# Performance work log

Hardware: AMD Instinct MI355X
Metric: run time of the kernel (lower is better)

Reference implementation:

```python
import jax, jax.numpy as jnp
import numpy as np

BATCH, NODES, ENC, DEC = 8192, 1_000_000, 128, 128


def setup_inputs() -> dict:
    key = jax.random.key(0)
    k1, k2, k3, k4 = jax.random.split(key, 4)
    query = jax.random.normal(k1, (BATCH, DEC), dtype=jnp.float32)
    values = jax.random.normal(k2, (NODES, ENC), dtype=jnp.float32)
    index = jax.random.randint(k3, (NODES,), 0, BATCH)
    W = jax.random.uniform(k4, (DEC, ENC), dtype=jnp.float32)
    return {"query": query, "values": values, "index": index, "W": W}


def reference(query, values, index, W):
    # query: [B, Ddec], values: [N, Denc], index: [N] in [0, B), W: [Ddec, Denc]
    batch = query.shape[0]
    dec = W.shape[0]
    # Original computes scores = query @ (W @ values.T) -> [B, N], then
    # scatter_softmax per segment along nodes, then gathers weights[index[n], n].
    # Only the row index[n] of column n is ever used, so we compute exactly
    # those entries: s[n] = <query[index[n]] @ W, values[n]> / sqrt(dec).
    qW = query @ W                                   # [B, Denc]
    s = jnp.einsum("ne,ne->n", qW[index], values)    # [N]
    s = s / jnp.sqrt(jnp.asarray(dec, dtype=s.dtype))
    # segment-wise stable softmax over nodes within each segment
    smax = jax.ops.segment_max(s, index, num_segments=batch)   # [B]
    e = jnp.exp(s - smax[index])                               # [N]
    denom = jax.ops.segment_sum(e, index, num_segments=batch)  # [B]
    w = e / denom[index]                                       # [N]
    # weighted scatter-add pooling -> [B, Denc]
    return jax.ops.segment_sum(w[:, None] * values, index, num_segments=batch)
```

## Files before the change

### kernel.cpp

```cpp
#include <hip/hip_runtime.h>
#include <hip/hip_bf16.h>
#include <cmath>

#define ENCD 128
#define DECD 128
#define CHUNK 32

__global__ void init_counts(int* __restrict__ counts, int B) {
    int i = blockIdx.x * blockDim.x + threadIdx.x;
    if (i < B) counts[i] = 0;
}

__global__ void qw_gemm(const float* __restrict__ query, const float* __restrict__ W,
                        float* __restrict__ qW) {
    __shared__ float qs[8][DECD];
    const int t = threadIdx.x;
    const int row0 = blockIdx.x * 8;
    for (int i = t; i < 8 * DECD; i += 256)
        qs[i >> 7][i & 127] = query[(size_t)row0 * DECD + i];
    __syncthreads();
    const int c = t & 127;
    const int rh = t >> 7;
    float a0 = 0.f, a1 = 0.f, a2 = 0.f, a3 = 0.f;
    for (int k = 0; k < DECD; ++k) {
        const float w = W[k * ENCD + c];
        a0 += qs[rh * 4 + 0][k] * w;
        a1 += qs[rh * 4 + 1][k] * w;
        a2 += qs[rh * 4 + 2][k] * w;
        a3 += qs[rh * 4 + 3][k] * w;
    }
    qW[(size_t)(row0 + rh * 4 + 0) * ENCD + c] = a0;
    qW[(size_t)(row0 + rh * 4 + 1) * ENCD + c] = a1;
    qW[(size_t)(row0 + rh * 4 + 2) * ENCD + c] = a2;
    qW[(size_t)(row0 + rh * 4 + 3) * ENCD + c] = a3;
}

__global__ void hist_kernel(const int* __restrict__ index, int* __restrict__ counts, int N) {
    int n4 = (blockIdx.x * blockDim.x + threadIdx.x) * 4;
    if (n4 + 3 < N) {
        const int4 v = *(const int4*)(index + n4);
        atomicAdd(&counts[v.x], 1);
        atomicAdd(&counts[v.y], 1);
        atomicAdd(&counts[v.z], 1);
        atomicAdd(&counts[v.w], 1);
    } else {
        for (int n = n4; n < N; ++n) atomicAdd(&counts[index[n]], 1);
    }
}

__global__ void scan_kernel(const int* __restrict__ counts, int* __restrict__ offsets,
                            int* __restrict__ cursor, int B) {
    __shared__ int tot[1024];
    const int t = threadIdx.x;
    int local[8];
    int s = 0;
#pragma unroll
    for (int i = 0; i < 8; ++i) {
        const int ci = t * 8 + i;
        local[i] = (ci < B) ? counts[ci] : 0;
        s += local[i];
    }
    tot[t] = s;
    __syncthreads();
    for (int off = 1; off < 1024; off <<= 1) {
        int v = (t >= off) ? tot[t - off] : 0;
        __syncthreads();
        tot[t] += v;
        __syncthreads();
    }
    int excl = tot[t] - s;
#pragma unroll
    for (int i = 0; i < 8; ++i) {
        const int ci = t * 8 + i;
        if (ci < B) { offsets[ci] = excl; cursor[ci] = excl; }
        excl += local[i];
    }
    if (t == 1023) offsets[B] = tot[1023];
}

__global__ void scatter_kernel(const int* __restrict__ index, int* __restrict__ cursor,
                               int* __restrict__ nodeids, int N) {
    int n = blockIdx.x * blockDim.x + threadIdx.x;
    if (n < N) {
        const int p = atomicAdd(&cursor[index[n]], 1);
        nodeids[p] = n;
    }
}

__global__ __launch_bounds__(256) void seg_attn(
    const float* __restrict__ values, const float* __restrict__ qW,
    const int* __restrict__ offsets, const int* __restrict__ nodeids,
    float* __restrict__ out) {
    const int b = blockIdx.x;
    const int t = threadIdx.x;
    const int beg = offsets[b];
    const int cnt = offsets[b + 1] - beg;

    __shared__ float qsh[ENCD];
    __shared__ float vrow[CHUNK][ENCD + 4];
    __shared__ float s_sh[CHUNK];
    __shared__ int   nid_sh[CHUNK];
    __shared__ float mrg_a[ENCD];
    __shared__ float mrg_l[ENCD];

    if (t < ENCD) qsh[t] = qW[(size_t)b * ENCD + t];
    __syncthreads();

    const int g  = t & 15;
    const int jn = t >> 4;
    float qreg[8];
#pragma unroll
    for (int i = 0; i < 8; ++i) qreg[i] = qsh[g * 8 + i];

    const int col  = t & 127;
    const int half = t >> 7;

    float m = -INFINITY, l = 0.f, acc = 0.f;
    const float inv_sqrt_d = 0.08838834764831845f;

    for (int base = 0; base < cnt; base += CHUNK) {
        const int nim = min(CHUNK, cnt - base);
        if (t < CHUNK) nid_sh[t] = nodeids[beg + ((t < nim) ? (base + t) : base)];
        __syncthreads();

        {
            const int r0 = t >> 5;
            const int c4 = (t & 31) * 4;
#pragma unroll
            for (int it = 0; it < 4; ++it) {
                const int r = r0 + it * 8;
                const float4 v = *(const float4*)(values + (size_t)nid_sh[r] * ENCD + c4);
                *(float4*)&vrow[r][c4] = v;
            }
        }
        __syncthreads();

#pragma unroll
        for (int p = 0; p < 2; ++p) {
            const int j = jn + p * 16;
            float pd = 0.f;
#pragma unroll
            for (int i = 0; i < 8; ++i) pd += qreg[i] * vrow[j][g * 8 + i];
            pd += __shfl_xor(pd, 1);
            pd += __shfl_xor(pd, 2);
            pd += __shfl_xor(pd, 4);
            pd += __shfl_xor(pd, 8);
            if (g == 0) s_sh[j] = (j < nim) ? pd * inv_sqrt_d : -INFINITY;
        }
        __syncthreads();

        float m_ch = -INFINITY;
#pragma unroll
        for (int j = 0; j < CHUNK; ++j) m_ch = fmaxf(m_ch, s_sh[j]);
        const float m_new = fmaxf(m, m_ch);
        const float scale = __expf(m - m_new);
        float psum = 0.f, accadd = 0.f;
#pragma unroll
        for (int jj = 0; jj < 16; ++jj) {
            const int j = half * 16 + jj;
            const float p = __expf(s_sh[j] - m_new);
            psum += p;
            accadd += p * vrow[j][col];
        }
        l = l * scale + psum;
        acc = acc * scale + accadd;
        m = m_new;
    }

    if (half == 1) { mrg_a[col] = acc; mrg_l[col] = l; }
    __syncthreads();
    if (half == 0) {
        const float at = acc + mrg_a[col];
        const float lt = l + mrg_l[col];
        out[(size_t)b * ENCD + col] = (lt > 0.f) ? (at / lt) : 0.f;
    }
}

extern "C" void kernel_launch(void* const* d_in, const int* in_sizes, int n_in,
                              void* d_out, int out_size, void* d_ws, size_t ws_size,
                              hipStream_t stream) {
    const float* query  = (const float*)d_in[0];
    const float* values = (const float*)d_in[1];
    const int*   index  = (const int*)d_in[2];
    const float* W      = (const float*)d_in[3];
    float* out = (float*)d_out;

    const int B = in_sizes[0] / DECD;
    const int N = in_sizes[2];

    float* qW      = (float*)d_ws;
    int*   nodeids = (int*)(qW + (size_t)B * ENCD);
    int*   counts  = nodeids + N;
    int*   offsets = counts + B;
    int*   cursor  = offsets + B + 1;

    init_counts<<<(B + 255) / 256, 256, 0, stream>>>(counts, B);
    qw_gemm<<<B / 8, 256, 0, stream>>>(query, W, qW);
    hist_kernel<<<(N / 4 + 255) / 256, 256, 0, stream>>>(index, counts, N);
    scan_kernel<<<1, 1024, 0, stream>>>(counts, offsets, cursor, B);
    scatter_kernel<<<(N + 255) / 256, 256, 0, stream>>>(index, cursor, nodeids, N);
    seg_attn<<<B, 256, 0, stream>>>(values, qW, offsets, nodeids, out);
}
```

Before: 839.8 us.

## Restructure segment attention into per-wavefront online softmax with register prefetch

The segment attention kernel now gives each of the four wavefronts its own stream of 8 nodes per step. Each wavefront keeps its own running max, sum and accumulator, and double-buffers the next node rows in registers, so no block-wide barriers are needed inside the loop. The four partial softmax states are merged at the end with rescaling. The scatter kernel also handles four indices per thread using int4 loads. The cost is more registers per thread and per-wave LDS use, and each wavefront processes only 8 nodes per iteration, which may leave work unbalanced when segments are short.

```diff
diff --git a/kernel.cpp b/kernel.cpp
--- a/kernel.cpp
+++ b/kernel.cpp
@@ -1,10 +1,9 @@
 #include <hip/hip_runtime.h>
-#include <hip/hip_bf16.h>
 #include <cmath>
 
 #define ENCD 128
 #define DECD 128
-#define CHUNK 32
+#define INV_SQRT_D 0.08838834764831845f
 
 __global__ void init_counts(int* __restrict__ counts, int B) {
     int i = blockIdx.x * blockDim.x + threadIdx.x;
@@ -80,12 +79,67 @@
 
 __global__ void scatter_kernel(const int* __restrict__ index, int* __restrict__ cursor,
                                int* __restrict__ nodeids, int N) {
-    int n = blockIdx.x * blockDim.x + threadIdx.x;
-    if (n < N) {
-        const int p = atomicAdd(&cursor[index[n]], 1);
-        nodeids[p] = n;
-    }
-}
+    int n4 = (blockIdx.x * blockDim.x + threadIdx.x) * 4;
+    if (n4 + 3 < N) {
+        const int4 v = *(const int4*)(index + n4);
+        const int p0 = atomicAdd(&cursor[v.x], 1); nodeids[p0] = n4 + 0;
+        const int p1 = atomicAdd(&cursor[v.y], 1); nodeids[p1] = n4 + 1;
+        const int p2 = atomicAdd(&cursor[v.z], 1); nodeids[p2] = n4 + 2;
+        const int p3 = atomicAdd(&cursor[v.w], 1); nodeids[p3] = n4 + 3;
+    } else {
+        for (int n = n4; n < N; ++n) {
+            const int p = atomicAdd(&cursor[index[n]], 1);
+            nodeids[p] = n;
+        }
+    }
+}
+
+__device__ __forceinline__ float dot4(const float4 a, const float4 b) {
+    return a.x * b.x + a.y * b.y + a.z * b.z + a.w * b.w;
+}
+
+#define SEG_ITER(CUR, NXT, P)                                                  \
+  {                                                                            \
+    float pd = dot4(CUR[0], q4[0]) + dot4(CUR[1], q4[1]) +                     \
+               dot4(CUR[2], q4[2]) + dot4(CUR[3], q4[3]);                      \
+    pd += __shfl_xor(pd, 8);                                                   \
+    pd += __shfl_xor(pd, 16);                                                  \
+    pd += __shfl_xor(pd, 32);                                                  \
+    const float sc = ((P) + r < end) ? pd * INV_SQRT_D : -INFINITY;            \
+    float mc = sc;                                                             \
+    mc = fmaxf(mc, __shfl_xor(mc, 1));                                         \
+    mc = fmaxf(mc, __shfl_xor(mc, 2));                                         \
+    mc = fmaxf(mc, __shfl_xor(mc, 4));                                         \
+    const float m_new = fmaxf(m, mc);      \
+    const float scale = __expf(m - m_new);        \
+    const float pe = __expf(sc - m_new);        \
+    float* dst = &vsh[w][r][g * 16];                                           \
+    *(float4*)(dst + 0)  = CUR[0];                                             \
+    *(float4*)(dst + 4)  = CUR[1];                                             \
+    *(float4*)(dst + 8)  = CUR[2];                                             \
+    *(float4*)(dst + 12) = CUR[3];                                             \
+    if ((P) + 32 < end) {                              \
+      const float* vp = values + (size_t)nid_next * ENCD + g * 16;             \
+      NXT[0] = *(const float4*)(vp + 0);                                       \
+      NXT[1] = *(const float4*)(vp + 4);                                       \
+      NXT[2] = *(const float4*)(vp + 8);                                       \
+      NXT[3] = *(const float4*)(vp + 12);                                      \
+      const int nn = (P) + 64 + r;                                             \
+      nid_next = nodeids[(nn < end) ? nn : beg];                               \
+    }                                                                          \
+    float psum = 0.f, ad0 = 0.f, ad1 = 0.f;                                    \
+    _Pragma("unroll")                                                          \
+    for (int j = 0; j < 8; ++j) {                                              \
+      const float pj = __shfl(pe, j);           \
+      psum += pj;                                                              \
+      ad0 += pj * vsh[w][j][l];        \
+      ad1 += pj * vsh[w][j][l + 64];                                           \
+    }                                                                          \
+    acc0 = acc0 * scale + ad0;                                                 \
+    acc1 = acc1 * scale + ad1;                                                 \
+    lacc = lacc * scale + psum;                                                \
+    m = m_new;                                                                 \
+  }
 
 __global__ __launch_bounds__(256) void seg_attn(
     const float* __restrict__ values, const float* __restrict__ qW,
@@ -93,86 +147,67 @@
     float* __restrict__ out) {
     const int b = blockIdx.x;
     const int t = threadIdx.x;
+    const int w = t >> 6;
+    const int l = t & 63;
+    const int r = l & 7;
+    const int g = l >> 3;
+
     const int beg = offsets[b];
-    const int cnt = offsets[b + 1] - beg;
-
-    __shared__ float qsh[ENCD];
-    __shared__ float vrow[CHUNK][ENCD + 4];
-    __shared__ float s_sh[CHUNK];
-    __shared__ int   nid_sh[CHUNK];
-    __shared__ float mrg_a[ENCD];
-    __shared__ float mrg_l[ENCD];
-
-    if (t < ENCD) qsh[t] = qW[(size_t)b * ENCD + t];
+    const int end = offsets[b + 1];
+
+    __shared__ float vsh[4][8][ENCD + 4];
+    __shared__ float mrg_a[4][ENCD];
+    __shared__ float mrg_l[4];
+    __shared__ float mrg_m[4];
+
+    float4 q4[4];
+#pragma unroll
+    for (int i = 0; i < 4; ++i)
+        q4[i] = *(const float4*)(qW + (size_t)b * ENCD + g * 16 + i * 4);
+
+    float acc0 = 0.f, acc1 = 0.f, lacc = 0.f;
+    float m = -INFINITY;
+    float4 va[4], vb[4];
+    int nid_next = 0;
+
+    int p = beg + w * 8;
+    if (p < end) {
+        {
+            const int pp = p + r;
+            const int nid0 = nodeids[(pp < end) ? pp : beg];
+            const float* vp = values + (size_t)nid0 * ENCD + g * 16;
+            va[0] = *(const float4*)(vp + 0);
+            va[1] = *(const float4*)(vp + 4);
+            va[2] = *(const float4*)(vp + 8);
+            va[3] = *(const float4*)(vp + 12);
+            const int np = p + 32 + r;
+            nid_next = nodeids[(np < end) ? np : beg];
+        }
+        while (true) {
+            SEG_ITER(va, vb, p);
+            p += 32;
+            if (p >= end) break;
+            SEG_ITER(vb, va, p);
+            p += 32;
+            if (p >= end) break;
+        }
+    }
+
+    mrg_a[w][l] = acc0;
+    mrg_a[w][l + 64] = acc1;
+    if (l == 0) { mrg_l[w] = lacc; mrg_m[w] = m; }
     __syncthreads();
-
-    const int g  = t & 15;
-    const int jn = t >> 4;
-    float qreg[8];
-#pragma unroll
-    for (int i = 0; i < 8; ++i) qreg[i] = qsh[g * 8 + i];
-
-    const int col  = t & 127;
-    const int half = t >> 7;
-
-    float m = -INFINITY, l = 0.f, acc = 0.f;
-    const float inv_sqrt_d = 0.08838834764831845f;
-
-    for (int base = 0; base < cnt; base += CHUNK) {
-        const int nim = min(CHUNK, cnt - base);
-        if (t < CHUNK) nid_sh[t] = nodeids[beg + ((t < nim) ? (base + t) : base)];
-        __syncthreads();
-
-        {
-            const int r0 = t >> 5;
-            const int c4 = (t & 31) * 4;
-#pragma unroll
-            for (int it = 0; it < 4; ++it) {
-                const int r = r0 + it * 8;
-                const float4 v = *(const float4*)(values + (size_t)nid_sh[r] * ENCD + c4);
-                *(float4*)&vrow[r][c4] = v;
-            }
-        }
-        __syncthreads();
-
-#pragma unroll
-        for (int p = 0; p < 2; ++p) {
-            const int j = jn + p * 16;
-            float pd = 0.f;
-#pragma unroll
-            for (int i = 0; i < 8; ++i) pd += qreg[i] * vrow[j][g * 8 + i];
-            pd += __shfl_xor(pd, 1);
-            pd += __shfl_xor(pd, 2);
-            pd += __shfl_xor(pd, 4);
-            pd += __shfl_xor(pd, 8);
-            if (g == 0) s_sh[j] = (j < nim) ? pd * inv_sqrt_d : -INFINITY;
-        }
-        __syncthreads();
-
-        float m_ch = -INFINITY;
-#pragma unroll
-        for (int j = 0; j < CHUNK; ++j) m_ch = fmaxf(m_ch, s_sh[j]);
-        const float m_new = fmaxf(m, m_ch);
-        const float scale = __expf(m - m_new);
-        float psum = 0.f, accadd = 0.f;
-#pragma unroll
-        for (int jj = 0; jj < 16; ++jj) {
-            const int j = half * 16 + jj;
-            const float p = __expf(s_sh[j] - m_new);
-            psum += p;
-            accadd += p * vrow[j][col];
-        }
-        l = l * scale + psum;
-        acc = acc * scale + accadd;
-        m = m_new;
-    }
-
-    if (half == 1) { mrg_a[col] = acc; mrg_l[col] = l; }
-    __syncthreads();
-    if (half == 0) {
-        const float at = acc + mrg_a[col];
-        const float lt = l + mrg_l[col];
-        out[(size_t)b * ENCD + col] = (lt > 0.f) ? (at / lt) : 0.f;
+    if (t < ENCD) {
+        const float mt = fmaxf(fmaxf(mrg_m[0], mrg_m[1]), fmaxf(mrg_m[2], mrg_m[3]));
+        float a = 0.f, lt = 0.f;
+#pragma unroll
+        for (int ww = 0; ww < 4; ++ww) {
+            const float mw = mrg_m[ww];
+            const float rs = (mw == mt) ? 1.f : __expf(mw - mt);
+            a += rs * mrg_a[ww][t];
+            lt += rs * mrg_l[ww];
+        }
+        out[(size_t)b * ENCD + t] = (lt > 0.f) ? (a / lt) : 0.f;
     }
 }
 
@@ -198,6 +233,6 @@
     qw_gemm<<<B / 8, 256, 0, stream>>>(query, W, qW);
     hist_kernel<<<(N / 4 + 255) / 256, 256, 0, stream>>>(index, counts, N);
     scan_kernel<<<1, 1024, 0, stream>>>(counts, offsets, cursor, B);
-    scatter_kernel<<<(N + 255) / 256, 256, 0, stream>>>(index, cursor, nodeids, N);
+    scatter_kernel<<<(N / 4 + 255) / 256, 256, 0, stream>>>(index, cursor, nodeids, N);
     seg_attn<<<B, 256, 0, stream>>>(values, qW, offsets, nodeids, out);
 }
```

After: 833.2 us. No clear change (-0.8%).
